# Kernel optimization log

Measured on AMD Instinct MI355X. Metric: run time of the kernel, lower is better.

## Reference

```python
import jax, jax.numpy as jnp
import numpy as np

N_NODES = 100000
N_EDGES = 1600000
LN_EPS = 1e-5
CLAMP = 1.8


def setup_inputs() -> dict:
    key = jax.random.key(0)
    ks = jax.random.split(key, 12)
    feats = [100, 64, 64, 47]
    inp = {
        "x": jax.random.normal(ks[0], (N_NODES, feats[0]), dtype=jnp.float32),
        "adj_vals": jax.random.uniform(ks[1], (N_EDGES,), dtype=jnp.float32),
        "adj_row": jax.random.randint(ks[2], (N_EDGES,), 0, N_NODES),
        "adj_col": jax.random.randint(ks[3], (N_EDGES,), 0, N_NODES),
        "ln_gamma": jnp.ones((feats[0],), dtype=jnp.float32),
        "ln_beta": jnp.zeros((feats[0],), dtype=jnp.float32),
    }
    for i in range(3):
        fi, fo = feats[i], feats[i + 1]
        bound = 1.0 / np.sqrt(fi)
        inp[f"W{i+1}"] = jax.random.uniform(ks[4 + 2 * i], (fi, fo), minval=-bound, maxval=bound, dtype=jnp.float32)
        inp[f"b{i+1}"] = jax.random.uniform(ks[5 + 2 * i], (fo,), minval=-bound, maxval=bound, dtype=jnp.float32)
    return inp


def _spmm(vals, row, col, x):
    # out[i] = sum_{e: row[e]==i} vals[e] * x[col[e]]
    gathered = vals[:, None] * x[col]  # [E, D]
    return jax.ops.segment_sum(gathered, row, num_segments=N_NODES)


def reference(x, adj_vals, adj_row, adj_col, ln_gamma, ln_beta, W1, b1, W2, b2, W3, b3):
    # clamp to [-1.8, 1.8]: relu(x+1.8)-1.8 then 1.8-relu(1.8-x)
    x = jnp.clip(x, -CLAMP, CLAMP)
    # LayerNorm over last dim (100)
    mu = jnp.mean(x, axis=-1, keepdims=True)
    var = jnp.mean(jnp.square(x - mu), axis=-1, keepdims=True)
    x = (x - mu) * jax.lax.rsqrt(var + LN_EPS) * ln_gamma + ln_beta
    # GCN layers: Linear -> spmm -> (elu except last); dropout=0 => identity
    x = jax.nn.elu(_spmm(adj_vals, adj_row, adj_col, x @ W1 + b1))
    x = jax.nn.elu(_spmm(adj_vals, adj_row, adj_col, x @ W2 + b2))
    x = _spmm(adj_vals, adj_row, adj_col, x @ W3 + b3)
    return x
```

## Files before the change

### kernel.cpp

```cpp
#include <hip/hip_runtime.h>
#include <cstdint>
#include <cstddef>

#define N_NODES_C 100000
#define N_EDGES_C 1600000
#define LN_EPS_C 1e-5f
#define CLAMP_C 1.8f

__device__ __forceinline__ float readlane_f(float v, int l) {
  return __uint_as_float(__builtin_amdgcn_readlane(__float_as_uint(v), l));
}

__device__ __forceinline__ float wave_sum(float v) {
#pragma unroll
  for (int off = 32; off > 0; off >>= 1) v += __shfl_xor(v, off, 64);
  return v;
}

__global__ void hist_kernel(const int* __restrict__ row, int* __restrict__ counts) {
  int stride = gridDim.x * blockDim.x;
  for (int e = blockIdx.x * blockDim.x + threadIdx.x; e < N_EDGES_C; e += stride)
    atomicAdd(&counts[row[e]], 1);
}

__global__ void scan1_kernel(const int* __restrict__ counts, int* __restrict__ rowstart,
                             int* __restrict__ bsums) {
  __shared__ int lds[256];
  int t = threadIdx.x;
  int base = blockIdx.x * 1024 + t * 4;
  int c0 = (base + 0 < N_NODES_C) ? counts[base + 0] : 0;
  int c1 = (base + 1 < N_NODES_C) ? counts[base + 1] : 0;
  int c2 = (base + 2 < N_NODES_C) ? counts[base + 2] : 0;
  int c3 = (base + 3 < N_NODES_C) ? counts[base + 3] : 0;
  int s = c0 + c1 + c2 + c3;
  lds[t] = s;
  __syncthreads();
#pragma unroll
  for (int off = 1; off < 256; off <<= 1) {
    int v = (t >= off) ? lds[t - off] : 0;
    __syncthreads();
    lds[t] += v;
    __syncthreads();
  }
  int incl = lds[t];
  int excl = incl - s;
  if (t == 255) bsums[blockIdx.x] = incl;
  if (base + 0 < N_NODES_C) rowstart[base + 0] = excl;
  excl += c0;
  if (base + 1 < N_NODES_C) rowstart[base + 1] = excl;
  excl += c1;
  if (base + 2 < N_NODES_C) rowstart[base + 2] = excl;
  excl += c2;
  if (base + 3 < N_NODES_C) rowstart[base + 3] = excl;
}

__global__ void scan2_kernel(int* __restrict__ bsums, int nb) {
  __shared__ int lds[128];
  int t = threadIdx.x;
  int v = (t < nb) ? bsums[t] : 0;
  lds[t] = v;
  __syncthreads();
#pragma unroll
  for (int off = 1; off < 128; off <<= 1) {
    int u = (t >= off) ? lds[t - off] : 0;
    __syncthreads();
    lds[t] += u;
    __syncthreads();
  }
  if (t < nb) bsums[t] = lds[t] - v;
}

__global__ void scan3_kernel(int* __restrict__ rowstart, int* __restrict__ cursor,
                             const int* __restrict__ bsums) {
  int add = bsums[blockIdx.x];
  int base = blockIdx.x * 1024 + threadIdx.x * 4;
#pragma unroll
  for (int i = 0; i < 4; ++i)
    if (base + i < N_NODES_C) {
      int v = rowstart[base + i] + add;
      rowstart[base + i] = v;
      cursor[base + i] = v;
    }
}

__global__ __launch_bounds__(256) void scatter_kernel(
    const int* __restrict__ row, const int* __restrict__ col,
    const float* __restrict__ vals, int* __restrict__ cursor,
    int2* __restrict__ edges_s) {
  int tid = blockIdx.x * blockDim.x + threadIdx.x;
  int nt = gridDim.x * blockDim.x;
  int r[8], c[8], p[8];
  float v[8];
#pragma unroll
  for (int k = 0; k < 8; ++k) {
    int e = tid + k * nt;
    bool in = e < N_EDGES_C;
    r[k] = in ? row[e] : 0;
    c[k] = in ? col[e] : 0;
    v[k] = in ? vals[e] : 0.f;
  }
#pragma unroll
  for (int k = 0; k < 8; ++k) {
    int e = tid + k * nt;
    if (e < N_EDGES_C) p[k] = atomicAdd(&cursor[r[k]], 1);
  }
#pragma unroll
  for (int k = 0; k < 8; ++k) {
    int e = tid + k * nt;
    if (e < N_EDGES_C) edges_s[p[k]] = make_int2(c[k], __float_as_int(v[k]));
  }
}

__global__ __launch_bounds__(256) void ln_gemm1_kernel(
    const float* __restrict__ x, const float* __restrict__ gamma, const float* __restrict__ beta,
    const float* __restrict__ W1, const float* __restrict__ b1, float* __restrict__ y) {
  int lane = threadIdx.x & 63;
  int wid = blockIdx.x * (blockDim.x >> 6) + (threadIdx.x >> 6);
  int nw = gridDim.x * (blockDim.x >> 6);
  float w[100];
#pragma unroll
  for (int k = 0; k < 100; ++k) w[k] = W1[k * 64 + lane];
  float bias = b1[lane];
  float g0 = gamma[lane];
  float be0 = beta[lane];
  float g1 = (lane < 36) ? gamma[64 + lane] : 0.f;
  float be1 = (lane < 36) ? beta[64 + lane] : 0.f;
  for (int n = wid; n < N_NODES_C; n += nw) {
    const float* xr = x + (size_t)n * 100;
    float x0 = xr[lane];
    float x1 = (lane < 36) ? xr[64 + lane] : 0.f;
    x0 = fminf(fmaxf(x0, -CLAMP_C), CLAMP_C);
    x1 = fminf(fmaxf(x1, -CLAMP_C), CLAMP_C);
    float mu = wave_sum(x0 + x1) * 0.01f;
    float d0 = x0 - mu;
    float d1 = (lane < 36) ? (x1 - mu) : 0.f;
    float var = wave_sum(d0 * d0 + d1 * d1) * 0.01f;
    float inv = rsqrtf(var + LN_EPS_C);
    float xn0 = d0 * inv * g0 + be0;
    float xn1 = d1 * inv * g1 + be1;
    float acc = bias;
#pragma unroll
    for (int k = 0; k < 64; ++k) acc = fmaf(readlane_f(xn0, k), w[k], acc);
#pragma unroll
    for (int k = 0; k < 36; ++k) acc = fmaf(readlane_f(xn1, k), w[64 + k], acc);
    y[(size_t)n * 64 + lane] = acc;
  }
}

template <int DOUT, int OPITCH>
__global__ __launch_bounds__(256) void spmm_elu_gemm_kernel(
    const int* __restrict__ rowstart, const int* __restrict__ counts,
    const int2* __restrict__ edges_s, const float* __restrict__ y,
    const float* __restrict__ W, const float* __restrict__ b, float* __restrict__ out) {
  int lane = threadIdx.x & 63;
  int wid = blockIdx.x * (blockDim.x >> 6) + (threadIdx.x >> 6);
  int nw = gridDim.x * (blockDim.x >> 6);
  float w[64];
#pragma unroll
  for (int k = 0; k < 64; ++k) w[k] = (lane < DOUT) ? W[k * DOUT + lane] : 0.f;
  float bias = (lane < DOUT) ? b[lane] : 0.f;
  for (int n = wid; n < N_NODES_C; n += nw) {
    int start = rowstart[n];
    int cnt = counts[n];
    float a0 = 0.f, a1 = 0.f, a2 = 0.f, a3 = 0.f, a4 = 0.f, a5 = 0.f, a6 = 0.f, a7 = 0.f;
    for (int base = 0; base < cnt; base += 64) {
      int m = cnt - base;
      if (m > 64) m = 64;
      int2 ev = make_int2(0, 0);
      if (lane < m) ev = edges_s[start + base + lane];
      int mr = (m + 7) & ~7;
      for (int j = 0; j < mr; j += 8) {
        float g0 = y[(size_t)__builtin_amdgcn_readlane(ev.x, j + 0) * 64 + lane];
        float g1 = y[(size_t)__builtin_amdgcn_readlane(ev.x, j + 1) * 64 + lane];
        float g2 = y[(size_t)__builtin_amdgcn_readlane(ev.x, j + 2) * 64 + lane];
        float g3 = y[(size_t)__builtin_amdgcn_readlane(ev.x, j + 3) * 64 + lane];
        float g4 = y[(size_t)__builtin_amdgcn_readlane(ev.x, j + 4) * 64 + lane];
        float g5 = y[(size_t)__builtin_amdgcn_readlane(ev.x, j + 5) * 64 + lane];
        float g6 = y[(size_t)__builtin_amdgcn_readlane(ev.x, j + 6) * 64 + lane];
        float g7 = y[(size_t)__builtin_amdgcn_readlane(ev.x, j + 7) * 64 + lane];
        a0 = fmaf(__uint_as_float(__builtin_amdgcn_readlane((unsigned)ev.y, j + 0)), g0, a0);
        a1 = fmaf(__uint_as_float(__builtin_amdgcn_readlane((unsigned)ev.y, j + 1)), g1, a1);
        a2 = fmaf(__uint_as_float(__builtin_amdgcn_readlane((unsigned)ev.y, j + 2)), g2, a2);
        a3 = fmaf(__uint_as_float(__builtin_amdgcn_readlane((unsigned)ev.y, j + 3)), g3, a3);
        a4 = fmaf(__uint_as_float(__builtin_amdgcn_readlane((unsigned)ev.y, j + 4)), g4, a4);
        a5 = fmaf(__uint_as_float(__builtin_amdgcn_readlane((unsigned)ev.y, j + 5)), g5, a5);
        a6 = fmaf(__uint_as_float(__builtin_amdgcn_readlane((unsigned)ev.y, j + 6)), g6, a6);
        a7 = fmaf(__uint_as_float(__builtin_amdgcn_readlane((unsigned)ev.y, j + 7)), g7, a7);
      }
    }
    float acc = ((a0 + a1) + (a2 + a3)) + ((a4 + a5) + (a6 + a7));
    float xe = (acc > 0.f) ? acc : expm1f(acc);
    float o = bias;
#pragma unroll
    for (int k = 0; k < 64; ++k) o = fmaf(readlane_f(xe, k), w[k], o);
    if (lane < DOUT) out[(size_t)n * OPITCH + lane] = o;
  }
}

__global__ __launch_bounds__(256) void spmm_final_kernel(
    const int* __restrict__ rowstart, const int* __restrict__ counts,
    const int2* __restrict__ edges_s, const float* __restrict__ y,
    float* __restrict__ out) {
  int lane = threadIdx.x & 63;
  int wid = blockIdx.x * (blockDim.x >> 6) + (threadIdx.x >> 6);
  int nw = gridDim.x * (blockDim.x >> 6);
  int lmask = (lane < 47) ? lane : 46;
  for (int n = wid; n < N_NODES_C; n += nw) {
    int start = rowstart[n];
    int cnt = counts[n];
    float a0 = 0.f, a1 = 0.f, a2 = 0.f, a3 = 0.f, a4 = 0.f, a5 = 0.f, a6 = 0.f, a7 = 0.f;
    for (int base = 0; base < cnt; base += 64) {
      int m = cnt - base;
      if (m > 64) m = 64;
      int2 ev = make_int2(0, 0);
      if (lane < m) ev = edges_s[start + base + lane];
      int mr = (m + 7) & ~7;
      for (int j = 0; j < mr; j += 8) {
        float g0 = y[(size_t)__builtin_amdgcn_readlane(ev.x, j + 0) * 48 + lmask];
        float g1 = y[(size_t)__builtin_amdgcn_readlane(ev.x, j + 1) * 48 + lmask];
        float g2 = y[(size_t)__builtin_amdgcn_readlane(ev.x, j + 2) * 48 + lmask];
        float g3 = y[(size_t)__builtin_amdgcn_readlane(ev.x, j + 3) * 48 + lmask];
        float g4 = y[(size_t)__builtin_amdgcn_readlane(ev.x, j + 4) * 48 + lmask];
        float g5 = y[(size_t)__builtin_amdgcn_readlane(ev.x, j + 5) * 48 + lmask];
        float g6 = y[(size_t)__builtin_amdgcn_readlane(ev.x, j + 6) * 48 + lmask];
        float g7 = y[(size_t)__builtin_amdgcn_readlane(ev.x, j + 7) * 48 + lmask];
        a0 = fmaf(__uint_as_float(__builtin_amdgcn_readlane((unsigned)ev.y, j + 0)), g0, a0);
        a1 = fmaf(__uint_as_float(__builtin_amdgcn_readlane((unsigned)ev.y, j + 1)), g1, a1);
        a2 = fmaf(__uint_as_float(__builtin_amdgcn_readlane((unsigned)ev.y, j + 2)), g2, a2);
        a3 = fmaf(__uint_as_float(__builtin_amdgcn_readlane((unsigned)ev.y, j + 3)), g3, a3);
        a4 = fmaf(__uint_as_float(__builtin_amdgcn_readlane((unsigned)ev.y, j + 4)), g4, a4);
        a5 = fmaf(__uint_as_float(__builtin_amdgcn_readlane((unsigned)ev.y, j + 5)), g5, a5);
        a6 = fmaf(__uint_as_float(__builtin_amdgcn_readlane((unsigned)ev.y, j + 6)), g6, a6);
        a7 = fmaf(__uint_as_float(__builtin_amdgcn_readlane((unsigned)ev.y, j + 7)), g7, a7);
      }
    }
    float acc = ((a0 + a1) + (a2 + a3)) + ((a4 + a5) + (a6 + a7));
    if (lane < 47) out[(size_t)n * 47 + lane] = acc;
  }
}

extern "C" void kernel_launch(void* const* d_in, const int* in_sizes, int n_in,
                              void* d_out, int out_size, void* d_ws, size_t ws_size,
                              hipStream_t stream) {
  const float* x = (const float*)d_in[0];
  const float* adj_vals = (const float*)d_in[1];
  const int* adj_row = (const int*)d_in[2];
  const int* adj_col = (const int*)d_in[3];
  const float* gamma = (const float*)d_in[4];
  const float* beta = (const float*)d_in[5];
  const float* W1 = (const float*)d_in[6];
  const float* b1 = (const float*)d_in[7];
  const float* W2 = (const float*)d_in[8];
  const float* b2 = (const float*)d_in[9];
  const float* W3 = (const float*)d_in[10];
  const float* b3 = (const float*)d_in[11];
  float* out = (float*)d_out;

  char* ws = (char*)d_ws;
  size_t off = 0;
  auto alloc = [&](size_t bytes) -> void* {
    void* p = ws + off;
    off += (bytes + 255) & ~(size_t)255;
    return p;
  };
  float* bufA = (float*)alloc(sizeof(float) * (size_t)N_NODES_C * 64);
  float* bufB = (float*)alloc(sizeof(float) * (size_t)N_NODES_C * 64);
  int* counts = (int*)alloc(sizeof(int) * N_NODES_C);
  int* cursor = (int*)alloc(sizeof(int) * N_NODES_C);
  int* rowstart = (int*)alloc(sizeof(int) * N_NODES_C);
  int* bsums = (int*)alloc(sizeof(int) * 256);
  int2* edges_s = (int2*)alloc(sizeof(int2) * N_EDGES_C);

  hipMemsetAsync(counts, 0, sizeof(int) * N_NODES_C, stream);

  hist_kernel<<<2048, 256, 0, stream>>>(adj_row, counts);
  int nb = (N_NODES_C + 1023) / 1024;
  scan1_kernel<<<nb, 256, 0, stream>>>(counts, rowstart, bsums);
  scan2_kernel<<<1, 128, 0, stream>>>(bsums, nb);
  scan3_kernel<<<nb, 256, 0, stream>>>(rowstart, cursor, bsums);
  scatter_kernel<<<1024, 256, 0, stream>>>(adj_row, adj_col, adj_vals, cursor, edges_s);

  ln_gemm1_kernel<<<1024, 256, 0, stream>>>(x, gamma, beta, W1, b1, bufA);
  spmm_elu_gemm_kernel<64, 64><<<2048, 256, 0, stream>>>(rowstart, counts, edges_s, bufA,
                                                         W2, b2, bufB);
  spmm_elu_gemm_kernel<47, 48><<<2048, 256, 0, stream>>>(rowstart, counts, edges_s, bufB,
                                                         W3, b3, bufA);
  spmm_final_kernel<<<2048, 256, 0, stream>>>(rowstart, counts, edges_s, bufA, out);
}
```

Measured before the change: 472.9 us.

## Store intermediate features in bf16 and fuse scatter with LayerNorm-GEMM1 launch

Intermediate node-feature buffers are now stored as bf16 (round-to-nearest-even) instead of fp32, which halves the bytes moved by the random row gathers in each SpMM. The edge scatter and the LayerNorm+GEMM1 stage are merged into one launch with block-range specialization, so the two independent jobs can run at the same time. Accumulation stays in fp32. The cost is reduced precision in the intermediates, which risks tolerance failures. The scatter path also picks up the 100-register weight-array footprint of the LN branch, which may lower its occupancy.

```diff
diff --git a/kernel.cpp b/kernel.cpp
--- a/kernel.cpp
+++ b/kernel.cpp
@@ -6,6 +6,10 @@
 #define N_EDGES_C 1600000
 #define LN_EPS_C 1e-5f
 #define CLAMP_C 1.8f
+#define SC_BLOCKS 1024
+#define LN_BLOCKS 1024
+
+typedef unsigned short ushort_t;
 
 __device__ __forceinline__ float readlane_f(float v, int l) {
   return __uint_as_float(__builtin_amdgcn_readlane(__float_as_uint(v), l));
@@ -15,6 +19,15 @@
 #pragma unroll
   for (int off = 32; off > 0; off >>= 1) v += __shfl_xor(v, off, 64);
   return v;
+}
+
+__device__ __forceinline__ ushort_t f2bf(float f) {
+  unsigned u = __float_as_uint(f);
+  unsigned r = (u + 0x7fffu + ((u >> 16) & 1u)) >> 16;
+  return (ushort_t)r;
+}
+__device__ __forceinline__ float bf2f(ushort_t u) {
+  return __uint_as_float((unsigned)u << 16);
 }
 
 __global__ void hist_kernel(const int* __restrict__ row, int* __restrict__ counts) {
@@ -83,75 +96,77 @@
     }
 }
 
-__global__ __launch_bounds__(256) void scatter_kernel(
+__global__ __launch_bounds__(256) void scatter_ln_kernel(
     const int* __restrict__ row, const int* __restrict__ col,
     const float* __restrict__ vals, int* __restrict__ cursor,
-    int2* __restrict__ edges_s) {
-  int tid = blockIdx.x * blockDim.x + threadIdx.x;
-  int nt = gridDim.x * blockDim.x;
-  int r[8], c[8], p[8];
-  float v[8];
-#pragma unroll
-  for (int k = 0; k < 8; ++k) {
-    int e = tid + k * nt;
-    bool in = e < N_EDGES_C;
-    r[k] = in ? row[e] : 0;
-    c[k] = in ? col[e] : 0;
-    v[k] = in ? vals[e] : 0.f;
-  }
-#pragma unroll
-  for (int k = 0; k < 8; ++k) {
-    int e = tid + k * nt;
-    if (e < N_EDGES_C) p[k] = atomicAdd(&cursor[r[k]], 1);
-  }
-#pragma unroll
-  for (int k = 0; k < 8; ++k) {
-    int e = tid + k * nt;
-    if (e < N_EDGES_C) edges_s[p[k]] = make_int2(c[k], __float_as_int(v[k]));
-  }
-}
-
-__global__ __launch_bounds__(256) void ln_gemm1_kernel(
-    const float* __restrict__ x, const float* __restrict__ gamma, const float* __restrict__ beta,
-    const float* __restrict__ W1, const float* __restrict__ b1, float* __restrict__ y) {
-  int lane = threadIdx.x & 63;
-  int wid = blockIdx.x * (blockDim.x >> 6) + (threadIdx.x >> 6);
-  int nw = gridDim.x * (blockDim.x >> 6);
-  float w[100];
-#pragma unroll
-  for (int k = 0; k < 100; ++k) w[k] = W1[k * 64 + lane];
-  float bias = b1[lane];
-  float g0 = gamma[lane];
-  float be0 = beta[lane];
-  float g1 = (lane < 36) ? gamma[64 + lane] : 0.f;
-  float be1 = (lane < 36) ? beta[64 + lane] : 0.f;
-  for (int n = wid; n < N_NODES_C; n += nw) {
-    const float* xr = x + (size_t)n * 100;
-    float x0 = xr[lane];
-    float x1 = (lane < 36) ? xr[64 + lane] : 0.f;
-    x0 = fminf(fmaxf(x0, -CLAMP_C), CLAMP_C);
-    x1 = fminf(fmaxf(x1, -CLAMP_C), CLAMP_C);
-    float mu = wave_sum(x0 + x1) * 0.01f;
-    float d0 = x0 - mu;
-    float d1 = (lane < 36) ? (x1 - mu) : 0.f;
-    float var = wave_sum(d0 * d0 + d1 * d1) * 0.01f;
-    float inv = rsqrtf(var + LN_EPS_C);
-    float xn0 = d0 * inv * g0 + be0;
-    float xn1 = d1 * inv * g1 + be1;
-    float acc = bias;
-#pragma unroll
-    for (int k = 0; k < 64; ++k) acc = fmaf(readlane_f(xn0, k), w[k], acc);
-#pragma unroll
-    for (int k = 0; k < 36; ++k) acc = fmaf(readlane_f(xn1, k), w[64 + k], acc);
-    y[(size_t)n * 64 + lane] = acc;
-  }
-}
-
-template <int DOUT, int OPITCH>
+    int2* __restrict__ edges_s,
+    const float* __restrict__ x, const float* __restrict__ gamma,
+    const float* __restrict__ beta, const float* __restrict__ W1,
+    const float* __restrict__ b1, ushort_t* __restrict__ y) {
+  if (blockIdx.x < SC_BLOCKS) {
+    int tid = blockIdx.x * 256 + threadIdx.x;
+    const int nt = SC_BLOCKS * 256;
+    int r[8], c[8], p[8];
+    float v[8];
+#pragma unroll
+    for (int k = 0; k < 8; ++k) {
+      int e = tid + k * nt;
+      bool in = e < N_EDGES_C;
+      r[k] = in ? row[e] : 0;
+      c[k] = in ? col[e] : 0;
+      v[k] = in ? vals[e] : 0.f;
+    }
+#pragma unroll
+    for (int k = 0; k < 8; ++k) {
+      int e = tid + k * nt;
+      if (e < N_EDGES_C) p[k] = atomicAdd(&cursor[r[k]], 1);
+    }
+#pragma unroll
+    for (int k = 0; k < 8; ++k) {
+      int e = tid + k * nt;
+      if (e < N_EDGES_C) edges_s[p[k]] = make_int2(c[k], __float_as_int(v[k]));
+    }
+  } else {
+    int lane = threadIdx.x & 63;
+    int wid = (blockIdx.x - SC_BLOCKS) * 4 + (threadIdx.x >> 6);
+    const int nw = LN_BLOCKS * 4;
+    float w[100];
+#pragma unroll
+    for (int k = 0; k < 100; ++k) w[k] = W1[k * 64 + lane];
+    float bias = b1[lane];
+    float g0 = gamma[lane];
+    float be0 = beta[lane];
+    float g1 = (lane < 36) ? gamma[64 + lane] : 0.f;
+    float be1 = (lane < 36) ? beta[64 + lane] : 0.f;
+    for (int n = wid; n < N_NODES_C; n += nw) {
+      const float* xr = x + (size_t)n * 100;
+      float x0 = xr[lane];
+      float x1 = (lane < 36) ? xr[64 + lane] : 0.f;
+      x0 = fminf(fmaxf(x0, -CLAMP_C), CLAMP_C);
+      x1 = fminf(fmaxf(x1, -CLAMP_C), CLAMP_C);
+      float mu = wave_sum(x0 + x1) * 0.01f;
+      float d0 = x0 - mu;
+      float d1 = (lane < 36) ? (x1 - mu) : 0.f;
+      float var = wave_sum(d0 * d0 + d1 * d1) * 0.01f;
+      float inv = rsqrtf(var + LN_EPS_C);
+      float xn0 = d0 * inv * g0 + be0;
+      float xn1 = d1 * inv * g1 + be1;
+      float acc = bias;
+#pragma unroll
+      for (int k = 0; k < 64; ++k) acc = fmaf(readlane_f(xn0, k), w[k], acc);
+#pragma unroll
+      for (int k = 0; k < 36; ++k) acc = fmaf(readlane_f(xn1, k), w[64 + k], acc);
+      y[(size_t)n * 64 + lane] = f2bf(acc);
+    }
+  }
+}
+
+template <int DOUT>
 __global__ __launch_bounds__(256) void spmm_elu_gemm_kernel(
     const int* __restrict__ rowstart, const int* __restrict__ counts,
-    const int2* __restrict__ edges_s, const float* __restrict__ y,
-    const float* __restrict__ W, const float* __restrict__ b, float* __restrict__ out) {
+    const int2* __restrict__ edges_s, const ushort_t* __restrict__ yb,
+    const float* __restrict__ W, const float* __restrict__ b,
+    ushort_t* __restrict__ out) {
   int lane = threadIdx.x & 63;
   int wid = blockIdx.x * (blockDim.x >> 6) + (threadIdx.x >> 6);
   int nw = gridDim.x * (blockDim.x >> 6);
@@ -170,14 +185,14 @@
       if (lane < m) ev = edges_s[start + base + lane];
       int mr = (m + 7) & ~7;
       for (int j = 0; j < mr; j += 8) {
-        float g0 = y[(size_t)__builtin_amdgcn_readlane(ev.x, j + 0) * 64 + lane];
-        float g1 = y[(size_t)__builtin_amdgcn_readlane(ev.x, j + 1) * 64 + lane];
-        float g2 = y[(size_t)__builtin_amdgcn_readlane(ev.x, j + 2) * 64 + lane];
-        float g3 = y[(size_t)__builtin_amdgcn_readlane(ev.x, j + 3) * 64 + lane];
-        float g4 = y[(size_t)__builtin_amdgcn_readlane(ev.x, j + 4) * 64 + lane];
-        float g5 = y[(size_t)__builtin_amdgcn_readlane(ev.x, j + 5) * 64 + lane];
-        float g6 = y[(size_t)__builtin_amdgcn_readlane(ev.x, j + 6) * 64 + lane];
-        float g7 = y[(size_t)__builtin_amdgcn_readlane(ev.x, j + 7) * 64 + lane];
+        float g0 = bf2f(yb[(size_t)__builtin_amdgcn_readlane(ev.x, j + 0) * 64 + lane]);
+        float g1 = bf2f(yb[(size_t)__builtin_amdgcn_readlane(ev.x, j + 1) * 64 + lane]);
+        float g2 = bf2f(yb[(size_t)__builtin_amdgcn_readlane(ev.x, j + 2) * 64 + lane]);
+        float g3 = bf2f(yb[(size_t)__builtin_amdgcn_readlane(ev.x, j + 3) * 64 + lane]);
+        float g4 = bf2f(yb[(size_t)__builtin_amdgcn_readlane(ev.x, j + 4) * 64 + lane]);
+        float g5 = bf2f(yb[(size_t)__builtin_amdgcn_readlane(ev.x, j + 5) * 64 + lane]);
+        float g6 = bf2f(yb[(size_t)__builtin_amdgcn_readlane(ev.x, j + 6) * 64 + lane]);
+        float g7 = bf2f(yb[(size_t)__builtin_amdgcn_readlane(ev.x, j + 7) * 64 + lane]);
         a0 = fmaf(__uint_as_float(__builtin_amdgcn_readlane((unsigned)ev.y, j + 0)), g0, a0);
         a1 = fmaf(__uint_as_float(__builtin_amdgcn_readlane((unsigned)ev.y, j + 1)), g1, a1);
         a2 = fmaf(__uint_as_float(__builtin_amdgcn_readlane((unsigned)ev.y, j + 2)), g2, a2);
@@ -193,13 +208,13 @@
     float o = bias;
 #pragma unroll
     for (int k = 0; k < 64; ++k) o = fmaf(readlane_f(xe, k), w[k], o);
-    if (lane < DOUT) out[(size_t)n * OPITCH + lane] = o;
+    if (lane < DOUT) out[(size_t)n * 64 + lane] = f2bf(o);
   }
 }
 
 __global__ __launch_bounds__(256) void spmm_final_kernel(
     const int* __restrict__ rowstart, const int* __restrict__ counts,
-    const int2* __restrict__ edges_s, const float* __restrict__ y,
+    const int2* __restrict__ edges_s, const ushort_t* __restrict__ yb,
     float* __restrict__ out) {
   int lane = threadIdx.x & 63;
   int wid = blockIdx.x * (blockDim.x >> 6) + (threadIdx.x >> 6);
@@ -216,14 +231,14 @@
       if (lane < m) ev = edges_s[start + base + lane];
       int mr = (m + 7) & ~7;
       for (int j = 0; j < mr; j += 8) {
-        float g0 = y[(size_t)__builtin_amdgcn_readlane(ev.x, j + 0) * 48 + lmask];
-        float g1 = y[(size_t)__builtin_amdgcn_readlane(ev.x, j + 1) * 48 + lmask];
-        float g2 = y[(size_t)__builtin_amdgcn_readlane(ev.x, j + 2) * 48 + lmask];
-        float g3 = y[(size_t)__builtin_amdgcn_readlane(ev.x, j + 3) * 48 + lmask];
-        float g4 = y[(size_t)__builtin_amdgcn_readlane(ev.x, j + 4) * 48 + lmask];
-        float g5 = y[(size_t)__builtin_amdgcn_readlane(ev.x, j + 5) * 48 + lmask];
-        float g6 = y[(size_t)__builtin_amdgcn_readlane(ev.x, j + 6) * 48 + lmask];
-        float g7 = y[(size_t)__builtin_amdgcn_readlane(ev.x, j + 7) * 48 + lmask];
+        float g0 = bf2f(yb[(size_t)__builtin_amdgcn_readlane(ev.x, j + 0) * 64 + lmask]);
+        float g1 = bf2f(yb[(size_t)__builtin_amdgcn_readlane(ev.x, j + 1) * 64 + lmask]);
+        float g2 = bf2f(yb[(size_t)__builtin_amdgcn_readlane(ev.x, j + 2) * 64 + lmask]);
+        float g3 = bf2f(yb[(size_t)__builtin_amdgcn_readlane(ev.x, j + 3) * 64 + lmask]);
+        float g4 = bf2f(yb[(size_t)__builtin_amdgcn_readlane(ev.x, j + 4) * 64 + lmask]);
+        float g5 = bf2f(yb[(size_t)__builtin_amdgcn_readlane(ev.x, j + 5) * 64 + lmask]);
+        float g6 = bf2f(yb[(size_t)__builtin_amdgcn_readlane(ev.x, j + 6) * 64 + lmask]);
+        float g7 = bf2f(yb[(size_t)__builtin_amdgcn_readlane(ev.x, j + 7) * 64 + lmask]);
         a0 = fmaf(__uint_as_float(__builtin_amdgcn_readlane((unsigned)ev.y, j + 0)), g0, a0);
         a1 = fmaf(__uint_as_float(__builtin_amdgcn_readlane((unsigned)ev.y, j + 1)), g1, a1);
         a2 = fmaf(__uint_as_float(__builtin_amdgcn_readlane((unsigned)ev.y, j + 2)), g2, a2);
@@ -263,8 +278,8 @@
     off += (bytes + 255) & ~(size_t)255;
     return p;
   };
-  float* bufA = (float*)alloc(sizeof(float) * (size_t)N_NODES_C * 64);
-  float* bufB = (float*)alloc(sizeof(float) * (size_t)N_NODES_C * 64);
+  ushort_t* bufA = (ushort_t*)alloc(sizeof(ushort_t) * (size_t)N_NODES_C * 64);
+  ushort_t* bufB = (ushort_t*)alloc(sizeof(ushort_t) * (size_t)N_NODES_C * 64);
   int* counts = (int*)alloc(sizeof(int) * N_NODES_C);
   int* cursor = (int*)alloc(sizeof(int) * N_NODES_C);
   int* rowstart = (int*)alloc(sizeof(int) * N_NODES_C);
@@ -278,12 +293,13 @@
   scan1_kernel<<<nb, 256, 0, stream>>>(counts, rowstart, bsums);
   scan2_kernel<<<1, 128, 0, stream>>>(bsums, nb);
   scan3_kernel<<<nb, 256, 0, stream>>>(rowstart, cursor, bsums);
-  scatter_kernel<<<1024, 256, 0, stream>>>(adj_row, adj_col, adj_vals, cursor, edges_s);
-
-  ln_gemm1_kernel<<<1024, 256, 0, stream>>>(x, gamma, beta, W1, b1, bufA);
-  spmm_elu_gemm_kernel<64, 64><<<2048, 256, 0, stream>>>(rowstart, counts, edges_s, bufA,
-                                                         W2, b2, bufB);
-  spmm_elu_gemm_kernel<47, 48><<<2048, 256, 0, stream>>>(rowstart, counts, edges_s, bufB,
-                                                         W3, b3, bufA);
+
+  scatter_ln_kernel<<<SC_BLOCKS + LN_BLOCKS, 256, 0, stream>>>(
+      adj_row, adj_col, adj_vals, cursor, edges_s, x, gamma, beta, W1, b1, bufA);
+
+  spmm_elu_gemm_kernel<64><<<2048, 256, 0, stream>>>(rowstart, counts, edges_s, bufA,
+                                                     W2, b2, bufB);
+  spmm_elu_gemm_kernel<47><<<2048, 256, 0, stream>>>(rowstart, counts, edges_s, bufB,
+                                                     W3, b3, bufA);
   spmm_final_kernel<<<2048, 256, 0, stream>>>(rowstart, counts, edges_s, bufA, out);
 }
```

After: 450.4 us. -4.8%, faster.
